# Optimization experiments

Hardware: AMD Instinct MI355X
Metric: run time of the kernel (lower is better)

Reference implementation:

```python
import jax, jax.numpy as jnp
import numpy as np

B, C, H, W = 8, 192, 128, 128
HEADS = 4


def setup_inputs() -> dict:
    key = jax.random.key(0)
    ks = jax.random.split(key, 5)
    s = 0.02
    x = jax.random.normal(ks[0], (B, C, H, W), dtype=jnp.float32)
    qkv_w = jax.random.normal(ks[1], (3 * C, C), dtype=jnp.float32) * s   # 1x1 conv weight
    qkv_b = jnp.zeros((3 * C,), dtype=jnp.float32)
    dw_w = jax.random.normal(ks[2], (3 * C, 1, 3, 3), dtype=jnp.float32) * s  # depthwise 3x3
    dw_b = jnp.zeros((3 * C,), dtype=jnp.float32)
    temperature = jnp.ones((HEADS, 1, 1), dtype=jnp.float32)
    proj_w = jax.random.normal(ks[3], (C, C), dtype=jnp.float32) * s      # 1x1 conv weight
    proj_b = jnp.zeros((C,), dtype=jnp.float32)
    return {"x": x, "qkv_w": qkv_w, "qkv_b": qkv_b, "dw_w": dw_w,
            "dw_b": dw_b, "temperature": temperature, "proj_w": proj_w,
            "proj_b": proj_b}


def _l2norm(t):
    # matches F.normalize(t, dim=-1): t / max(||t||_2, 1e-12)
    n = jnp.sqrt(jnp.sum(t * t, axis=-1, keepdims=True))
    return t / jnp.maximum(n, 1e-12)


def reference(x, qkv_w, qkv_b, dw_w, dw_b, temperature, proj_w, proj_b):
    b, c, h, w = x.shape
    d = c // HEADS
    # 1x1 conv -> [B, 3C, H, W]
    qkv = jnp.einsum('oc,bchw->bohw', qkv_w, x) + qkv_b[None, :, None, None]
    # depthwise 3x3 conv (groups = 3C), padding=1
    qkv = jax.lax.conv_general_dilated(
        qkv, dw_w, window_strides=(1, 1), padding=((1, 1), (1, 1)),
        dimension_numbers=('NCHW', 'OIHW', 'NCHW'),
        feature_group_count=3 * c) + dw_b[None, :, None, None]
    q, k, v = jnp.split(qkv, 3, axis=1)
    hw = h * w
    q = _l2norm(q.reshape(b, HEADS, d, hw))
    k = _l2norm(k.reshape(b, HEADS, d, hw))
    v = v.reshape(b, HEADS, d, hw)
    # transposed attention: [B, heads, d, d]
    attn = jnp.einsum('bhdn,bhen->bhde', q, k) * temperature[None]
    attn = jax.nn.softmax(attn, axis=-1)
    out = jnp.einsum('bhde,bhen->bhdn', attn, v).reshape(b, c, h, w)
    return jnp.einsum('oc,bchw->bohw', proj_w, out) + proj_b[None, :, None, None]
```

## Files before the change

### kernel.cpp

```cpp
#include <hip/hip_runtime.h>
#include <hip/hip_bf16.h>

typedef __hip_bfloat16 bf16;

#define B_   8
#define C_   192
#define OC3  576
#define H_   128
#define W_   128
#define HW_  16384
#define HEADS_ 4
#define D_   48

typedef float f32x4 __attribute__((ext_vector_type(4)));
typedef __bf16 bf16x8 __attribute__((ext_vector_type(8)));
typedef __bf16 bf16x4 __attribute__((ext_vector_type(4)));

__device__ __forceinline__ float b2f(bf16 v) { return __bfloat162float(v); }

__device__ __forceinline__ void stv4(bf16* p, const f32x4& v, float bi) {
    bf16x4 o;
#pragma unroll
    for (int r = 0; r < 4; ++r) o[r] = (__bf16)(v[r] + bi);
    *reinterpret_cast<bf16x4*>(p) = o;
}
__device__ __forceinline__ void stv4(float* p, const f32x4& v, float bi) {
    f32x4 o;
#pragma unroll
    for (int r = 0; r < 4; ++r) o[r] = v[r] + bi;
    *reinterpret_cast<f32x4*>(p) = o;
}

__device__ __forceinline__ void llds16(const void* g, void* l) {
    __builtin_amdgcn_global_load_lds(
        (const __attribute__((address_space(1))) unsigned int*)g,
        (__attribute__((address_space(3))) unsigned int*)l, 16, 0, 0);
}

__global__ void cvt_w(const float* __restrict__ qkv_w, __bf16* __restrict__ Wq) {
    const int row = blockIdx.x, c = threadIdx.x;
    Wq[row * C_ + c] = (__bf16)qkv_w[row * C_ + c];
}

__global__ void tx_cvt(const float* __restrict__ x, __bf16* __restrict__ Xt) {
    const int p0 = blockIdx.x * 128;
    const int b  = blockIdx.z;
    __shared__ __bf16 LT[128 * 196];

    for (int idx = threadIdx.x; idx < C_ * 128; idx += 256) {
        int c = idx >> 7, pp = idx & 127;
        LT[pp * 196 + c] = (__bf16)x[((size_t)b * C_ + c) * HW_ + p0 + pp];
    }
    __syncthreads();
    for (int idx = threadIdx.x; idx < 128 * 48; idx += 256) {
        int pp = idx / 48, c4 = idx % 48;
        *(uint2*)&Xt[((size_t)b * HW_ + p0 + pp) * C_ + c4 * 4] =
            *(const uint2*)&LT[pp * 196 + c4 * 4];
    }
}

__global__ void vtx(const bf16* __restrict__ qkv2, __bf16* __restrict__ vt) {
    const int p0 = blockIdx.x * 128;
    const int b  = blockIdx.z;
    const bf16* vb = qkv2 + ((size_t)b * OC3 + 384) * HW_;
    __shared__ __bf16 LT[128 * 200];

    for (int idx = threadIdx.x; idx < C_ * 128; idx += 256) {
        int c = idx >> 7, pp = idx & 127;
        LT[pp * 200 + c] = *(const __bf16*)&vb[(size_t)c * HW_ + p0 + pp];
    }
    __syncthreads();
    for (int idx = threadIdx.x; idx < 128 * 48; idx += 256) {
        int pp = idx / 48, c4 = idx % 48;
        *(uint2*)&vt[((size_t)b * HW_ + p0 + pp) * C_ + c4 * 4] =
            *(const uint2*)&LT[pp * 200 + c4 * 4];
    }
}

template<typename TOut>
__global__ __launch_bounds__(256, 4) void mfma_gemm(
        const __bf16* __restrict__ Wp, const __bf16* __restrict__ Xt,
        const float* __restrict__ bias, TOut* __restrict__ Y,
        const int O, const int K, const size_t a_bstride) {
    const int tid  = threadIdx.x;
    const int wid  = tid >> 6, lane = tid & 63;
    const int lm   = lane & 15, qd = lane >> 4;
    const int p0   = blockIdx.x * 128;
    const int o0   = blockIdx.y * 128;
    const int b    = blockIdx.z;
    const int wo0  = (wid >> 1) * 64, wn0 = (wid & 1) * 64;

    const __bf16* Wb = Wp + a_bstride * b + (size_t)o0 * K;
    const __bf16* Xb = Xt + ((size_t)b * HW_ + p0) * K;

    __shared__ __bf16 As[2][4096];
    __shared__ __bf16 Bs[2][4096];

    f32x4 acc[4][4] = {};

    auto stage = [&](int buf, int k0) {
#pragma unroll
        for (int r = 0; r < 2; ++r) {
            const int slot = r * 256 + tid;
            const int row = slot & 127, k8 = slot >> 7;
            llds16(Wb + (size_t)row * K + k0 + k8 * 8,
                   &As[buf][(size_t)(r * 256 + wid * 64) * 8]);
            llds16(Xb + (size_t)row * K + k0 + k8 * 8,
                   &Bs[buf][(size_t)(r * 256 + wid * 64) * 8]);
        }
    };

    const int NT = K >> 5;

    stage(0, 0);
    asm volatile("s_waitcnt vmcnt(0)" ::: "memory");
    __builtin_amdgcn_s_barrier();
    __builtin_amdgcn_sched_barrier(0);

    for (int t = 0; t < NT; ++t) {
        const int cur = t & 1;
        if (t + 1 < NT) stage(cur ^ 1, (t + 1) * 32);

        bf16x8 af[4], bfr[4];
#pragma unroll
        for (int i = 0; i < 4; ++i)
            af[i] = *(const bf16x8*)&As[cur][(qd * 128 + wo0 + i * 16 + lm) * 8];
#pragma unroll
        for (int j = 0; j < 4; ++j)
            bfr[j] = *(const bf16x8*)&Bs[cur][(qd * 128 + wn0 + j * 16 + lm) * 8];
#pragma unroll
        for (int i = 0; i < 4; ++i)
#pragma unroll
            for (int j = 0; j < 4; ++j)
                acc[i][j] = __builtin_amdgcn_mfma_f32_16x16x32_bf16(
                    bfr[j], af[i], acc[i][j], 0, 0, 0);

        asm volatile("s_waitcnt vmcnt(0)" ::: "memory");
        __builtin_amdgcn_s_barrier();
        __builtin_amdgcn_sched_barrier(0);
    }

    TOut* Yb = Y + (size_t)b * O * HW_;
#pragma unroll
    for (int i = 0; i < 4; ++i) {
        const int o = o0 + wo0 + i * 16 + lm;
        if (o < O) {
            const float bi = bias[o];
#pragma unroll
            for (int j = 0; j < 4; ++j) {
                const int p = p0 + wn0 + j * 16 + qd * 4;
                stv4(&Yb[(size_t)o * HW_ + p], acc[i][j], bi);
            }
        }
    }
}

__device__ __forceinline__ void dw_load_row(const __bf16* plane, int yy, int x0,
                                            float* r) {
    if (yy < 0 || yy > 127) {
#pragma unroll
        for (int i = 0; i < 10; ++i) r[i] = 0.f;
        return;
    }
    const __bf16* row = plane + yy * 128;
    bf16x8 v = *(const bf16x8*)(row + x0);
    r[0] = (x0 > 0) ? (float)row[x0 - 1] : 0.f;
#pragma unroll
    for (int i = 0; i < 8; ++i) r[1 + i] = (float)v[i];
    r[9] = (x0 + 8 < 128) ? (float)row[x0 + 8] : 0.f;
}

__global__ __launch_bounds__(256) void dwconv_fused(
        const bf16* __restrict__ in, const float* __restrict__ w9,
        const float* __restrict__ bias, bf16* __restrict__ out,
        float* __restrict__ sumsq) {
    const int ch = blockIdx.x;
    const int b  = blockIdx.y;
    const int tid = threadIdx.x;
    const char* ib = (const char*)(in + ((size_t)b * OC3 + ch) * HW_);

    __shared__ __bf16 plane[16384];
    __shared__ float red[256];

    {
        const int wid = tid >> 6, lane = tid & 63;
        char* lbase = (char*)plane + wid * 8192;
        const char* gbase = ib + wid * 8192;
#pragma unroll
        for (int i = 0; i < 8; ++i)
            llds16(gbase + i * 1024 + lane * 16, lbase + i * 1024);
    }

    float wv[9];
#pragma unroll
    for (int i = 0; i < 9; ++i) wv[i] = w9[ch * 9 + i];
    const float bi = bias[ch];

    __syncthreads();

    const int x0 = (tid & 15) * 8;
    const int y0 = (tid >> 4) * 8;
    bf16* ob = out + ((size_t)b * OC3 + ch) * HW_;

    float r0[10], r1[10], r2[10];
    dw_load_row(plane, y0 - 1, x0, r0);
    dw_load_row(plane, y0,     x0, r1);

    float ss = 0.f;
#pragma unroll
    for (int yi = 0; yi < 8; ++yi) {
        dw_load_row(plane, y0 + yi + 1, x0, r2);
        bf16x8 st;
#pragma unroll
        for (int xx = 0; xx < 8; ++xx) {
            float o = bi;
#pragma unroll
            for (int dx = 0; dx < 3; ++dx) {
                o += wv[0 + dx] * r0[xx + dx];
                o += wv[3 + dx] * r1[xx + dx];
                o += wv[6 + dx] * r2[xx + dx];
            }
            ss += o * o;
            st[xx] = (__bf16)o;
        }
        *(bf16x8*)(ob + (y0 + yi) * 128 + x0) = st;
#pragma unroll
        for (int i = 0; i < 10; ++i) { r0[i] = r1[i]; r1[i] = r2[i]; }
    }

    red[tid] = ss;
    __syncthreads();
    for (int stx = 128; stx > 0; stx >>= 1) {
        if (tid < stx) red[tid] += red[tid + stx];
        __syncthreads();
    }
    if (tid == 0) sumsq[b * OC3 + ch] = red[0];
}

__global__ __launch_bounds__(256) void qk_mfma(const bf16* __restrict__ qkv2,
                                               float* __restrict__ Spart) {
    const int slice = blockIdx.x, h = blockIdx.y, b = blockIdx.z;
    const __bf16* qb = (const __bf16*)(qkv2 + ((size_t)b * OC3 + h * D_) * HW_);
    const __bf16* kb = (const __bf16*)(qkv2 + ((size_t)b * OC3 + 192 + h * D_) * HW_);

    __shared__ char smem[36864];
    __bf16* qs = (__bf16*)smem;
    __bf16* ks = (__bf16*)(smem + 13056);
    float*  red = (float*)smem;

    const int tid = threadIdx.x, wid = tid >> 6, lane = tid & 63;
    const int lm = lane & 15, qd = lane >> 4;
    const int kw0 = wid * 32;

    f32x4 acc[3][3] = {};

    for (int sub = 0; sub < 4; ++sub) {
        const int n0 = slice * 512 + sub * 128;
        __syncthreads();
        for (int t = tid; t < 768; t += 256) {
            int r = t >> 4, c8 = t & 15;
            *(bf16x8*)&qs[r * 136 + c8 * 8] =
                *(const bf16x8*)(qb + (size_t)r * HW_ + n0 + c8 * 8);
            *(bf16x8*)&ks[r * 136 + c8 * 8] =
                *(const bf16x8*)(kb + (size_t)r * HW_ + n0 + c8 * 8);
        }
        __syncthreads();

        bf16x8 af[3], bfr[3];
#pragma unroll
        for (int i = 0; i < 3; ++i)
            af[i] = *(const bf16x8*)&qs[(i * 16 + lm) * 136 + kw0 + qd * 8];
#pragma unroll
        for (int j = 0; j < 3; ++j)
            bfr[j] = *(const bf16x8*)&ks[(j * 16 + lm) * 136 + kw0 + qd * 8];
#pragma unroll
        for (int i = 0; i < 3; ++i)
#pragma unroll
            for (int j = 0; j < 3; ++j)
                acc[i][j] = __builtin_amdgcn_mfma_f32_16x16x32_bf16(
                    af[i], bfr[j], acc[i][j], 0, 0, 0);
    }

    __syncthreads();
    float* wb = red + wid * 2304;
#pragma unroll
    for (int i = 0; i < 3; ++i)
#pragma unroll
        for (int j = 0; j < 3; ++j)
#pragma unroll
            for (int r = 0; r < 4; ++r)
                wb[(i * 16 + qd * 4 + r) * 48 + j * 16 + lm] = acc[i][j][r];
    __syncthreads();

    float* outp = Spart + ((size_t)((b * HEADS_ + h) * 32 + slice)) * 2304;
    for (int t = tid; t < 2304; t += 256)
        outp[t] = red[t] + red[2304 + t] + red[4608 + t] + red[6912 + t];
}

__global__ void softmax48(const float* __restrict__ Spart, const float* __restrict__ sumsq,
                          const float* __restrict__ temp, float* __restrict__ A) {
    const int h = blockIdx.x, b = blockIdx.y;
    const int i = threadIdx.x;
    if (i >= 48) return;
    const float* sq = sumsq + b * OC3 + h * D_;
    const float* sk = sumsq + b * OC3 + 192 + h * D_;
    const float t = temp[h];
    const float* Sp = Spart + ((size_t)(b * HEADS_ + h) * 32) * 2304;

    const float rqi = 1.0f / fmaxf(sqrtf(sq[i]), 1e-12f);

    float s[48];
#pragma unroll
    for (int j = 0; j < 48; ++j) {
        float v = 0.f;
        for (int sl = 0; sl < 32; ++sl) v += Sp[sl * 2304 + i * 48 + j];
        s[j] = v * rqi * (1.0f / fmaxf(sqrtf(sk[j]), 1e-12f)) * t;
    }
    float m = -1e30f;
#pragma unroll
    for (int j = 0; j < 48; ++j) m = fmaxf(m, s[j]);
    float sum = 0.f;
#pragma unroll
    for (int j = 0; j < 48; ++j) { s[j] = expf(s[j] - m); sum += s[j]; }
    float inv = 1.0f / sum;
    float* Ao = A + ((size_t)(b * HEADS_ + h) * 48 + i) * 48;
#pragma unroll
    for (int j = 0; j < 48; ++j) Ao[j] = s[j] * inv;
}

__global__ void wfuse(const float* __restrict__ proj_w, const float* __restrict__ A,
                      __bf16* __restrict__ Wf) {
    const int o = blockIdx.x, b = blockIdx.y;
    const int cp = threadIdx.x;
    const int h = cp / 48, j = cp % 48;
    const float* wrow = proj_w + o * C_ + h * D_;
    const float* Ah = A + (size_t)(b * HEADS_ + h) * 2304;
    float s = 0.f;
#pragma unroll
    for (int i = 0; i < 48; ++i) s += wrow[i] * Ah[i * 48 + j];
    Wf[((size_t)b * 256 + o) * C_ + cp] = (__bf16)s;
}

extern "C" void kernel_launch(void* const* d_in, const int* in_sizes, int n_in,
                              void* d_out, int out_size, void* d_ws, size_t ws_size,
                              hipStream_t stream) {
    const float* x      = (const float*)d_in[0];
    const float* qkv_w  = (const float*)d_in[1];
    const float* qkv_b  = (const float*)d_in[2];
    const float* dw_w   = (const float*)d_in[3];
    const float* dw_b   = (const float*)d_in[4];
    const float* temp   = (const float*)d_in[5];
    const float* proj_w = (const float*)d_in[6];
    const float* proj_b = (const float*)d_in[7];
    float* out = (float*)d_out;

    char* ws = (char*)d_ws;
    const size_t XT_BYTES  = (size_t)B_ * HW_ * C_ * 2;
    const size_t WQ_BYTES  = 640 * C_ * 2;
    const size_t WF_BYTES  = (size_t)B_ * 256 * C_ * 2;
    const size_t QKV_BYTES = (size_t)B_ * OC3 * HW_ * 2;

    size_t off = 0;
    __bf16* Xt    = (__bf16*)(ws + off); off += XT_BYTES;
    __bf16* Wq    = (__bf16*)(ws + off); off += WQ_BYTES;
    __bf16* Wf    = (__bf16*)(ws + off); off += WF_BYTES;
    bf16*   bufA  = (bf16*)(ws + off);   off += QKV_BYTES;
    bf16*   bufB  = (bf16*)(ws + off);   off += QKV_BYTES;
    float*  sumsq = (float*)(ws + off);  off += OC3 * B_ * 4;
    float*  Spart = (float*)(ws + off);  off += (size_t)32 * 2304 * 4 * 32;
    float*  Attn  = (float*)(ws + off);  off += 294912;
    __bf16* vt    = Xt;

    cvt_w<<<dim3(OC3), 192, 0, stream>>>(qkv_w, Wq);

    tx_cvt<<<dim3(HW_ / 128, 1, B_), 256, 0, stream>>>(x, Xt);

    mfma_gemm<bf16><<<dim3(HW_ / 128, 5, B_), 256, 0, stream>>>(
        Wq, Xt, qkv_b, bufA, OC3, C_, 0);

    dwconv_fused<<<dim3(OC3, B_), 256, 0, stream>>>(bufA, dw_w, dw_b, bufB, sumsq);

    qk_mfma<<<dim3(32, HEADS_, B_), 256, 0, stream>>>(bufB, Spart);

    softmax48<<<dim3(HEADS_, B_), 64, 0, stream>>>(Spart, sumsq, temp, Attn);

    vtx<<<dim3(HW_ / 128, 1, B_), 256, 0, stream>>>(bufB, vt);

    wfuse<<<dim3(C_, B_), 192, 0, stream>>>(proj_w, Attn, Wf);

    mfma_gemm<float><<<dim3(HW_ / 128, 2, B_), 256, 0, stream>>>(
        Wf, vt, proj_b, out, C_, C_, (size_t)256 * C_);
}
```

Baseline: 478.9 us.

## Triple-buffer MFMA GEMM staging with swizzled LDS layout and compile-time K

```diff
diff --git a/kernel.cpp b/kernel.cpp
--- a/kernel.cpp
+++ b/kernel.cpp
@@ -77,11 +77,11 @@
     }
 }
 
-template<typename TOut>
+template<typename TOut, int KK>
 __global__ __launch_bounds__(256, 4) void mfma_gemm(
         const __bf16* __restrict__ Wp, const __bf16* __restrict__ Xt,
         const float* __restrict__ bias, TOut* __restrict__ Y,
-        const int O, const int K, const size_t a_bstride) {
+        const int O, const size_t a_bstride) {
     const int tid  = threadIdx.x;
     const int wid  = tid >> 6, lane = tid & 63;
     const int lm   = lane & 15, qd = lane >> 4;
@@ -90,54 +90,59 @@
     const int b    = blockIdx.z;
     const int wo0  = (wid >> 1) * 64, wn0 = (wid & 1) * 64;
 
-    const __bf16* Wb = Wp + a_bstride * b + (size_t)o0 * K;
-    const __bf16* Xb = Xt + ((size_t)b * HW_ + p0) * K;
-
-    __shared__ __bf16 As[2][4096];
-    __shared__ __bf16 Bs[2][4096];
+    const __bf16* Wb = Wp + a_bstride * b + (size_t)o0 * KK;
+    const __bf16* Xb = Xt + ((size_t)b * HW_ + p0) * KK;
+
+    __shared__ __bf16 As[3][4096];
+    __shared__ __bf16 Bs[3][4096];
 
     f32x4 acc[4][4] = {};
 
-    auto stage = [&](int buf, int k0) {
+    auto stage = [&](int buf, int t) {
+        const int k0 = t * 32;
 #pragma unroll
         for (int r = 0; r < 2; ++r) {
             const int slot = r * 256 + tid;
-            const int row = slot & 127, k8 = slot >> 7;
-            llds16(Wb + (size_t)row * K + k0 + k8 * 8,
+            const int row  = slot >> 2, cslot = slot & 3;
+            const int k8   = cslot ^ ((row >> 1) & 3);
+            llds16(Wb + (size_t)row * KK + k0 + k8 * 8,
                    &As[buf][(size_t)(r * 256 + wid * 64) * 8]);
-            llds16(Xb + (size_t)row * K + k0 + k8 * 8,
+            llds16(Xb + (size_t)row * KK + k0 + k8 * 8,
                    &Bs[buf][(size_t)(r * 256 + wid * 64) * 8]);
         }
     };
 
-    const int NT = K >> 5;
+    constexpr int NT = KK >> 5;
 
     stage(0, 0);
-    asm volatile("s_waitcnt vmcnt(0)" ::: "memory");
-    __builtin_amdgcn_s_barrier();
-    __builtin_amdgcn_sched_barrier(0);
-
+    stage(1, 1);
+
+    const int csl = qd ^ ((lm >> 1) & 3);
+
+#pragma unroll
     for (int t = 0; t < NT; ++t) {
-        const int cur = t & 1;
-        if (t + 1 < NT) stage(cur ^ 1, (t + 1) * 32);
-
+        __builtin_amdgcn_sched_barrier(0);
+        if (t < NT - 1) asm volatile("s_waitcnt vmcnt(4)" ::: "memory");
+        else            asm volatile("s_waitcnt vmcnt(0)" ::: "memory");
+        __builtin_amdgcn_s_barrier();
+        __builtin_amdgcn_sched_barrier(0);
+
+        if (t + 2 < NT) stage((t + 2) % 3, t + 2);
+
+        const int cur = t % 3;
         bf16x8 af[4], bfr[4];
 #pragma unroll
         for (int i = 0; i < 4; ++i)
-            af[i] = *(const bf16x8*)&As[cur][(qd * 128 + wo0 + i * 16 + lm) * 8];
+            af[i] = *(const bf16x8*)&As[cur][((wo0 + i * 16 + lm) * 4 + csl) * 8];
 #pragma unroll
         for (int j = 0; j < 4; ++j)
-            bfr[j] = *(const bf16x8*)&Bs[cur][(qd * 128 + wn0 + j * 16 + lm) * 8];
+            bfr[j] = *(const bf16x8*)&Bs[cur][((wn0 + j * 16 + lm) * 4 + csl) * 8];
 #pragma unroll
         for (int i = 0; i < 4; ++i)
 #pragma unroll
             for (int j = 0; j < 4; ++j)
                 acc[i][j] = __builtin_amdgcn_mfma_f32_16x16x32_bf16(
                     bfr[j], af[i], acc[i][j], 0, 0, 0);
-
-        asm volatile("s_waitcnt vmcnt(0)" ::: "memory");
-        __builtin_amdgcn_s_barrier();
-        __builtin_amdgcn_sched_barrier(0);
     }
 
     TOut* Yb = Y + (size_t)b * O * HW_;
@@ -375,8 +380,8 @@
 
     tx_cvt<<<dim3(HW_ / 128, 1, B_), 256, 0, stream>>>(x, Xt);
 
-    mfma_gemm<bf16><<<dim3(HW_ / 128, 5, B_), 256, 0, stream>>>(
-        Wq, Xt, qkv_b, bufA, OC3, C_, 0);
+    mfma_gemm<bf16, C_><<<dim3(HW_ / 128, 5, B_), 256, 0, stream>>>(
+        Wq, Xt, qkv_b, bufA, OC3, 0);
 
     dwconv_fused<<<dim3(OC3, B_), 256, 0, stream>>>(bufA, dw_w, dw_b, bufB, sumsq);
 
@@ -388,6 +393,6 @@
 
     wfuse<<<dim3(C_, B_), 192, 0, stream>>>(proj_w, Attn, Wf);
 
-    mfma_gemm<float><<<dim3(HW_ / 128, 2, B_), 256, 0, stream>>>(
-        Wf, vt, proj_b, out, C_, C_, (size_t)256 * C_);
-}
+    mfma_gemm<float, C_><<<dim3(HW_ / 128, 2, B_), 256, 0, stream>>>(
+        Wf, vt, proj_b, out, C_, (size_t)256 * C_);
+}
```

After: 444.7 us. 7.2% less time.
